# Kernel optimization log

Measured on AMD Instinct MI355X. Metric: run time of the kernel, lower is better.

## Reference

```python
import jax, jax.numpy as jnp
import numpy as np

B, S, D, H = 2, 2048, 1024, 16
DK = D // H


def setup_inputs() -> dict:
    key = jax.random.key(0)
    ks = jax.random.split(key, 12)
    s = 1.0 / np.sqrt(D)
    inp = {
        "query": jax.random.normal(ks[0], (B, S, D), jnp.float32),
        "key_": jax.random.normal(ks[1], (B, S, D), jnp.float32),
        "value": jax.random.normal(ks[2], (B, S, D), jnp.float32),
        # causal mask, broadcast over heads: [B, 1, S, S]
        "mask": jnp.broadcast_to(jnp.tril(jnp.ones((S, S), bool)), (B, 1, S, S)),
        "W_q": jax.random.uniform(ks[3], (D, D), jnp.float32, -s, s),
        "b_q": jax.random.uniform(ks[4], (D,), jnp.float32, -s, s),
        "W_k": jax.random.uniform(ks[5], (D, D), jnp.float32, -s, s),
        "b_k": jax.random.uniform(ks[6], (D,), jnp.float32, -s, s),
        "W_v": jax.random.uniform(ks[7], (D, D), jnp.float32, -s, s),
        "b_v": jax.random.uniform(ks[8], (D,), jnp.float32, -s, s),
        "W_o": jax.random.uniform(ks[9], (D, D), jnp.float32, -s, s),
        "b_o": jax.random.uniform(ks[10], (D,), jnp.float32, -s, s),
    }
    return inp


def reference(query, key_, value, mask, W_q, b_q, W_k, b_k, W_v, b_v, W_o, b_o):
    b = query.shape[0]
    # linear projections (torch Linear: x @ W.T + b)
    Q = query @ W_q.T + b_q
    K = key_ @ W_k.T + b_k
    V = value @ W_v.T + b_v
    # [b, S, H, dk] -> [b, H, S, dk]
    Q = Q.reshape(b, -1, H, DK).transpose(0, 2, 1, 3)
    K = K.reshape(b, -1, H, DK).transpose(0, 2, 1, 3)
    V = V.reshape(b, -1, H, DK).transpose(0, 2, 1, 3)
    scores = jnp.einsum("bhqd,bhkd->bhqk", Q, K) / jnp.sqrt(jnp.float32(DK))
    scores = jnp.where(mask, scores, -jnp.inf)
    attn = jax.nn.softmax(scores, axis=-1)
    out = jnp.einsum("bhqk,bhkd->bhqd", attn, V)
    out = out.transpose(0, 2, 1, 3).reshape(b, -1, D)
    return out @ W_o.T + b_o
```

## Files before the change

kernel.cpp:

```cpp
#include <hip/hip_runtime.h>
#include <hip/hip_bf16.h>
#include <stdint.h>

#define B_ 2
#define S_ 2048
#define D_ 1024
#define H_ 16
#define DK_ 64

typedef __attribute__((ext_vector_type(4))) float floatx4;
typedef __attribute__((ext_vector_type(8))) short shortx8;
typedef __attribute__((ext_vector_type(4))) short shortx4;
typedef unsigned short ushort_t;

__device__ inline ushort_t f2bf(float f) {
  union { float f; unsigned u; } v; v.f = f;
  unsigned r = v.u + 0x7FFFu + ((v.u >> 16) & 1u);
  return (ushort_t)(r >> 16);
}

__device__ inline unsigned pack2bf(float lo, float hi) {
  return __builtin_amdgcn_perm(__float_as_uint(hi), __float_as_uint(lo), 0x07060302u);
}

__device__ inline shortx4 mk_sx4(unsigned lo, unsigned hi) {
  union { unsigned u[2]; shortx4 s; } v; v.u[0] = lo; v.u[1] = hi; return v.s;
}

__device__ inline float fast_exp2(float x) {
#if __has_builtin(__builtin_amdgcn_exp2f)
  return __builtin_amdgcn_exp2f(x);
#else
  return __expf(0.69314718056f * x);
#endif
}

__device__ inline void gload_lds16(const void* g, void* l) {
  __builtin_amdgcn_global_load_lds(
      (const __attribute__((address_space(1))) unsigned int*)g,
      (__attribute__((address_space(3))) unsigned int*)l, 16, 0, 0);
}

__device__ inline floatx4 mfma16x16x16bf16(shortx4 a, shortx4 b, floatx4 c) {
#if __has_builtin(__builtin_amdgcn_mfma_f32_16x16x16bf16_1k)
  return __builtin_amdgcn_mfma_f32_16x16x16bf16_1k(a, b, c, 0, 0, 0);
#else
  floatx4 d;
  asm("v_mfma_f32_16x16x16_bf16 %0, %1, %2, %3" : "=v"(d) : "v"(a), "v"(b), "v"(c));
  return d;
#endif
}

struct ConvArgs {
  const float* src[7];
  ushort_t* dst[7];
};

__global__ __launch_bounds__(256) void convert_kernel(ConvArgs a) {
  int blk = blockIdx.x;
  int seg, bis;
  if (blk < 3072) { seg = blk >> 10; bis = blk & 1023; }
  else { int bb = blk - 3072; seg = 3 + (bb >> 8); bis = bb & 255; }
  const float4* src = (const float4*)(a.src[seg]) + (size_t)bis * 1024;
  ushort4* dst = (ushort4*)(a.dst[seg]) + (size_t)bis * 1024;
#pragma unroll
  for (int i = 0; i < 4; ++i) {
    int idx = i * 256 + threadIdx.x;
    float4 v = src[idx];
    ushort4 o;
    o.x = f2bf(v.x); o.y = f2bf(v.y); o.z = f2bf(v.z); o.w = f2bf(v.w);
    dst[idx] = o;
  }
}

template <int TM>
__device__ inline void gemm_bt_core(const ushort_t* __restrict__ A,
                                    const ushort_t* __restrict__ W,
                                    const float* __restrict__ bias,
                                    float scl,
                                    void* __restrict__ outp,
                                    int m0, int n0, int N, int K, int outmode) {
  constexpr int LDSU = (TM + 128) * 32;
  constexpr int GA = TM / 16;
  constexpr int GW = (GA + 8) / 4;
  constexpr int MI = TM / 32;
  __shared__ ushort_t smem[2][LDSU];
  const int tid = threadIdx.x;
  const int wave = tid >> 6;
  const int lane = tid & 63;
  const int quad = lane >> 4;
  const int l16 = lane & 15;
  const int wm = (wave >> 1) * (TM / 2);
  const int wn = (wave & 1) * 64;

  floatx4 acc[MI][4] = {};

  const ushort_t* gsrc[GW];
  int ldst[GW];
#pragma unroll
  for (int i = 0; i < GW; ++i) {
    int g = wave * GW + i;
    int row = lane >> 2;
    int col = (lane & 3) * 8;
    if (g < GA) {
      gsrc[i] = A + (size_t)(m0 + g * 16 + row) * K + col;
      ldst[i] = g * 512;
    } else {
      gsrc[i] = W + (size_t)(n0 + (g - GA) * 16 + row) * K + col;
      ldst[i] = TM * 32 + (g - GA) * 512;
    }
  }

#pragma unroll
  for (int i = 0; i < GW; ++i) gload_lds16(gsrc[i], &smem[0][ldst[i]]);

  const int niter = K >> 5;
  for (int j = 0; j < niter; ++j) {
    __syncthreads();
    if (j + 1 < niter) {
      const int ko = (j + 1) * 32;
      ushort_t* bufn = smem[(j + 1) & 1];
#pragma unroll
      for (int i = 0; i < GW; ++i) gload_lds16(gsrc[i] + ko, bufn + ldst[i]);
    }
    const ushort_t* aT = smem[j & 1];
    const ushort_t* bT = smem[j & 1] + TM * 32;
    shortx8 af[MI], bf[4];
#pragma unroll
    for (int mi = 0; mi < MI; ++mi)
      af[mi] = *(const shortx8*)(aT + (wm + mi * 16 + l16) * 32 + quad * 8);
#pragma unroll
    for (int ni = 0; ni < 4; ++ni)
      bf[ni] = *(const shortx8*)(bT + (wn + ni * 16 + l16) * 32 + quad * 8);
#pragma unroll
    for (int mi = 0; mi < MI; ++mi)
#pragma unroll
      for (int ni = 0; ni < 4; ++ni)
        acc[mi][ni] = __builtin_amdgcn_mfma_f32_16x16x32_bf16(af[mi], bf[ni], acc[mi][ni], 0, 0, 0);
  }

#pragma unroll
  for (int ni = 0; ni < 4; ++ni) {
    int n = n0 + wn + ni * 16 + l16;
    float bv = bias[n];
#pragma unroll
    for (int mi = 0; mi < MI; ++mi) {
      if (outmode == 2) {
        int m = m0 + wm + mi * 16 + quad * 4;
        int b = m >> 11, s = m & 2047;
        ushort_t* dst = (ushort_t*)outp + (((size_t)(b * 1024 + n)) << 11) + s;
        uint2 pk;
        pk.x = (unsigned)f2bf(acc[mi][ni][0] + bv) |
               ((unsigned)f2bf(acc[mi][ni][1] + bv) << 16);
        pk.y = (unsigned)f2bf(acc[mi][ni][2] + bv) |
               ((unsigned)f2bf(acc[mi][ni][3] + bv) << 16);
        *(uint2*)(dst) = pk;
      } else {
#pragma unroll
        for (int r = 0; r < 4; ++r) {
          int m = m0 + wm + mi * 16 + quad * 4 + r;
          float v = (acc[mi][ni][r] + bv) * scl;
          if (outmode == 1) ((float*)outp)[(size_t)m * N + n] = v;
          else ((ushort_t*)outp)[(size_t)m * N + n] = f2bf(v);
        }
      }
    }
  }
}

struct QkvArgs {
  const ushort_t* A[3];
  const ushort_t* W[3];
  const float* bias[3];
  ushort_t* out[3];
  float scale[3];
};

__global__ __launch_bounds__(256) void gemm_qkv_kernel(QkvArgs a) {
  int z = blockIdx.z;
  int m0 = (blockIdx.x * 4 + (blockIdx.y >> 3)) * 128;
  int n0 = (blockIdx.y & 7) * 128;
  gemm_bt_core<128>(a.A[z], a.W[z], a.bias[z], a.scale[z], a.out[z],
                    m0, n0, D_, D_, z == 2 ? 2 : 0);
}

__global__ __launch_bounds__(256) void gemm_out_kernel(const ushort_t* __restrict__ A,
                                                       const ushort_t* __restrict__ W,
                                                       const float* __restrict__ bias,
                                                       float* __restrict__ out) {
  int m0 = (blockIdx.x * 8 + (blockIdx.y >> 3)) * 64;
  int n0 = (blockIdx.y & 7) * 128;
  gemm_bt_core<64>(A, W, bias, 1.0f, out, m0, n0, D_, D_, 1);
}

__global__ __launch_bounds__(256, 2) void attn_kernel(const ushort_t* __restrict__ Qp,
                                                      const ushort_t* __restrict__ Kp,
                                                      const ushort_t* __restrict__ Vt,
                                                      ushort_t* __restrict__ O) {
  const int id = blockIdx.x;
  const int h = id & 15;
  const int qq = (id & 255) >> 4;
  const int b = id >> 8;
  const int qt = b ? qq : 15 - qq;
  const int q0 = qt * 128;
  const int tid = threadIdx.x;
  const int wave = tid >> 6;
  const int lane = tid & 63;
  const int quad = lane >> 4;
  const int l16 = lane & 15;

  __shared__ ushort_t smem[2][8192];

  const size_t hoff = (size_t)h * DK_;

  shortx8 qf[2][2];
#pragma unroll
  for (int grp = 0; grp < 2; ++grp) {
    const ushort_t* qrow = Qp + ((size_t)b * S_ + q0 + wave * 32 + grp * 16 + l16) * D_ + hoff;
#pragma unroll
    for (int ks = 0; ks < 2; ++ks)
      qf[grp][ks] = *(const shortx8*)(qrow + ks * 32 + quad * 8);
  }

  const int r8 = lane >> 3;
  const int jj8 = ((lane & 7) ^ r8) * 8;
  const ushort_t* kb[2];
  const ushort_t* vb[2];
#pragma unroll
  for (int g = 0; g < 2; ++g) {
    int r = wave * 16 + g * 8 + r8;
    kb[g] = Kp + ((size_t)b * S_ + r) * D_ + hoff + jj8;
    vb[g] = Vt + ((size_t)(b * H_ + h) * 64 + r) * S_ + jj8;
  }
  const int ldsrow = (wave * 16) * 64;

  floatx4 oacc[2][4] = {};
  float l_run[2] = {0.f, 0.f};
  const int nj = 2 * qt + 2;
  const int qwave_max = q0 + wave * 32 + 31;

#pragma unroll
  for (int g = 0; g < 2; ++g) {
    gload_lds16(kb[g], &smem[0][ldsrow + g * 512]);
    gload_lds16(vb[g], &smem[0][4096 + ldsrow + g * 512]);
  }

  for (int j = 0; j < nj; ++j) {
    __syncthreads();
    if (j + 1 < nj) {
      ushort_t* bufn = smem[(j + 1) & 1];
      const size_t ko = (size_t)(j + 1) * 64 * D_;
      const int vo = (j + 1) * 64;
#pragma unroll
      for (int g = 0; g < 2; ++g) {
        gload_lds16(kb[g] + ko, bufn + ldsrow + g * 512);
        gload_lds16(vb[g] + vo, bufn + 4096 + ldsrow + g * 512);
      }
    }
    if ((j << 6) > qwave_max) continue;
    const ushort_t* k_lds = smem[j & 1];
    const ushort_t* v_lds = smem[j & 1] + 4096;

    floatx4 sacc[2][4];
#pragma unroll
    for (int kkb = 0; kkb < 4; ++kkb) {
      const ushort_t* krow = k_lds + (kkb * 16 + l16) * 64;
      shortx8 af0 = *(const shortx8*)(krow + (quad ^ (l16 & 7)) * 8);
      shortx8 af1 = *(const shortx8*)(krow + ((4 | quad) ^ (l16 & 7)) * 8);
#pragma unroll
      for (int grp = 0; grp < 2; ++grp) {
        floatx4 acc = {0.f, 0.f, 0.f, 0.f};
        acc = __builtin_amdgcn_mfma_f32_16x16x32_bf16(af0, qf[grp][0], acc, 0, 0, 0);
        acc = __builtin_amdgcn_mfma_f32_16x16x32_bf16(af1, qf[grp][1], acc, 0, 0, 0);
        sacc[grp][kkb] = acc;
      }
    }
#pragma unroll
    for (int grp = 0; grp < 2; ++grp) {
      const int qg = q0 + wave * 32 + grp * 16 + l16;
      if ((j << 6) + 63 > q0 + wave * 32 + grp * 16) {
#pragma unroll
        for (int kkb = 0; kkb < 4; ++kkb)
#pragma unroll
          for (int r = 0; r < 4; ++r)
            if ((j << 6) + kkb * 16 + quad * 4 + r > qg) sacc[grp][kkb][r] = -3.0e38f;
      }
    }

    shortx4 pf[2][4];
#pragma unroll
    for (int grp = 0; grp < 2; ++grp) {
      float psum = 0.f;
#pragma unroll
      for (int kkb = 0; kkb < 4; ++kkb) {
        float p0 = fast_exp2(sacc[grp][kkb][0]);
        float p1 = fast_exp2(sacc[grp][kkb][1]);
        float p2 = fast_exp2(sacc[grp][kkb][2]);
        float p3 = fast_exp2(sacc[grp][kkb][3]);
        psum += (p0 + p1) + (p2 + p3);
        pf[grp][kkb] = mk_sx4(pack2bf(p0, p1), pack2bf(p2, p3));
      }
      l_run[grp] += psum;
    }

#pragma unroll
    for (int kkb = 0; kkb < 4; ++kkb) {
      const int jj = ((2 * kkb + (quad >> 1)) ^ (l16 & 7)) * 8 + (quad & 1) * 4;
#pragma unroll
      for (int db = 0; db < 4; ++db) {
        shortx4 vf = *(const shortx4*)(v_lds + (db * 16 + l16) * 64 + jj);
        oacc[0][db] = mfma16x16x16bf16(vf, pf[0][kkb], oacc[0][db]);
        oacc[1][db] = mfma16x16x16bf16(vf, pf[1][kkb], oacc[1][db]);
      }
    }
  }

  __syncthreads();
  ushort_t* sm = &smem[0][0];
#pragma unroll
  for (int grp = 0; grp < 2; ++grp) {
    float l0 = l_run[grp];
    l0 += __shfl_xor(l0, 16);
    l0 += __shfl_xor(l0, 32);
    float inv_l = 1.0f / l0;
    int row = wave * 32 + grp * 16 + l16;
#pragma unroll
    for (int db = 0; db < 4; ++db) {
#pragma unroll
      for (int rr = 0; rr < 2; ++rr) {
        unsigned pk = pack2bf(oacc[grp][db][rr * 2] * inv_l, oacc[grp][db][rr * 2 + 1] * inv_l);
        *(unsigned*)(sm + row * 72 + db * 16 + quad * 4 + rr * 2) = pk;
      }
    }
  }
  __syncthreads();
  {
    int r = tid >> 1, c = (tid & 1) * 32;
    const ushort_t* src = sm + r * 72 + c;
    ushort_t* dst = O + ((size_t)b * S_ + q0 + r) * D_ + hoff + c;
    uint4 v0 = *(const uint4*)(src);
    uint4 v1 = *(const uint4*)(src + 8);
    uint4 v2 = *(const uint4*)(src + 16);
    uint4 v3 = *(const uint4*)(src + 24);
    *(uint4*)(dst) = v0;
    *(uint4*)(dst + 8) = v1;
    *(uint4*)(dst + 16) = v2;
    *(uint4*)(dst + 24) = v3;
  }
}

extern "C" void kernel_launch(void* const* d_in, const int* in_sizes, int n_in,
                              void* d_out, int out_size, void* d_ws, size_t ws_size,
                              hipStream_t stream) {
  (void)in_sizes; (void)n_in; (void)out_size; (void)ws_size;
  char* ws = (char*)d_ws;
  ushort_t* xq = (ushort_t*)(ws + 0);
  ushort_t* xk = (ushort_t*)(ws + 8388608);
  ushort_t* xv = (ushort_t*)(ws + 16777216);
  ushort_t* wq = (ushort_t*)(ws + 25165824);
  ushort_t* wk = (ushort_t*)(ws + 27262976);
  ushort_t* wv = (ushort_t*)(ws + 29360128);
  ushort_t* wo = (ushort_t*)(ws + 31457280);
  ushort_t* Qp = (ushort_t*)(ws + 33554432);
  ushort_t* Kp = (ushort_t*)(ws + 41943040);
  ushort_t* Vt = (ushort_t*)(ws + 50331648);
  ushort_t* O = xq;

  ConvArgs ca;
  ca.src[0] = (const float*)d_in[0];  ca.dst[0] = xq;
  ca.src[1] = (const float*)d_in[1];  ca.dst[1] = xk;
  ca.src[2] = (const float*)d_in[2];  ca.dst[2] = xv;
  ca.src[3] = (const float*)d_in[4];  ca.dst[3] = wq;
  ca.src[4] = (const float*)d_in[6];  ca.dst[4] = wk;
  ca.src[5] = (const float*)d_in[8];  ca.dst[5] = wv;
  ca.src[6] = (const float*)d_in[10]; ca.dst[6] = wo;
  convert_kernel<<<dim3(4096), dim3(256), 0, stream>>>(ca);

  QkvArgs qa;
  qa.A[0] = xq; qa.W[0] = wq; qa.bias[0] = (const float*)d_in[5]; qa.out[0] = Qp;
  qa.A[1] = xk; qa.W[1] = wk; qa.bias[1] = (const float*)d_in[7]; qa.out[1] = Kp;
  qa.A[2] = xv; qa.W[2] = wv; qa.bias[2] = (const float*)d_in[9]; qa.out[2] = Vt;
  qa.scale[0] = 0.125f * 1.44269504089f;
  qa.scale[1] = 1.0f;
  qa.scale[2] = 1.0f;
  gemm_qkv_kernel<<<dim3(8, 32, 3), dim3(256), 0, stream>>>(qa);

  attn_kernel<<<dim3(512), dim3(256), 0, stream>>>(Qp, Kp, Vt, O);

  gemm_out_kernel<<<dim3(8, 64, 1), dim3(256), 0, stream>>>(
      O, wo, (const float*)d_in[11], (float*)d_out);
}
```

Before: 232.6 us.

## Fuse fp32-to-bf16 activation conversion into QKV GEMM loads

The QKV projection GEMM now reads the fp32 activations directly, converts them to bf16 in registers, and writes them to LDS. The separate conversion pass over the three input activation tensors is removed, leaving a smaller convert kernel that only handles the four weight matrices. This drops a full write and re-read of about 24 MB of bf16 activations. In exchange, the GEMM loads twice as many bytes for A per tile and spends VALU work on packing, and its launch bounds now ask for 3 blocks per CU. The output GEMM is specialised into a standalone kernel with the same tiling.

```diff
diff --git a/kernel.cpp b/kernel.cpp
--- a/kernel.cpp
+++ b/kernel.cpp
@@ -17,6 +17,13 @@
   union { float f; unsigned u; } v; v.f = f;
   unsigned r = v.u + 0x7FFFu + ((v.u >> 16) & 1u);
   return (ushort_t)(r >> 16);
+}
+
+__device__ inline unsigned pk_rne(float a, float b) {
+  unsigned ua = __float_as_uint(a), ub = __float_as_uint(b);
+  ua += 0x7FFFu + ((ua >> 16) & 1u);
+  ub += 0x7FFFu + ((ub >> 16) & 1u);
+  return __builtin_amdgcn_perm(ub, ua, 0x07060302u);
 }
 
 __device__ inline unsigned pack2bf(float lo, float hi) {
@@ -51,16 +58,13 @@
 #endif
 }
 
-struct ConvArgs {
-  const float* src[7];
-  ushort_t* dst[7];
+struct ConvWArgs {
+  const float* src[4];
+  ushort_t* dst[4];
 };
 
-__global__ __launch_bounds__(256) void convert_kernel(ConvArgs a) {
-  int blk = blockIdx.x;
-  int seg, bis;
-  if (blk < 3072) { seg = blk >> 10; bis = blk & 1023; }
-  else { int bb = blk - 3072; seg = 3 + (bb >> 8); bis = bb & 255; }
+__global__ __launch_bounds__(256) void convert_w_kernel(ConvWArgs a) {
+  int seg = blockIdx.x >> 8, bis = blockIdx.x & 255;
   const float4* src = (const float4*)(a.src[seg]) + (size_t)bis * 1024;
   ushort4* dst = (ushort4*)(a.dst[seg]) + (size_t)bis * 1024;
 #pragma unroll
@@ -73,70 +77,104 @@
   }
 }
 
-template <int TM>
-__device__ inline void gemm_bt_core(const ushort_t* __restrict__ A,
-                                    const ushort_t* __restrict__ W,
-                                    const float* __restrict__ bias,
-                                    float scl,
-                                    void* __restrict__ outp,
-                                    int m0, int n0, int N, int K, int outmode) {
-  constexpr int LDSU = (TM + 128) * 32;
-  constexpr int GA = TM / 16;
-  constexpr int GW = (GA + 8) / 4;
-  constexpr int MI = TM / 32;
-  __shared__ ushort_t smem[2][LDSU];
+struct QkvArgs {
+  const float* Af[3];
+  const ushort_t* W[3];
+  const float* bias[3];
+  ushort_t* out[3];
+  float scale[3];
+};
+
+__global__ __launch_bounds__(256, 3) void gemm_qkv_kernel(QkvArgs a) {
+  const int z = blockIdx.z;
+  const int m0 = (blockIdx.x * 4 + (blockIdx.y >> 3)) * 128;
+  const int n0 = (blockIdx.y & 7) * 128;
+  const float* __restrict__ A = a.Af[z];
+  const ushort_t* __restrict__ W = a.W[z];
+  const float* __restrict__ bias = a.bias[z];
+  const float scl = a.scale[z];
+  ushort_t* __restrict__ outp = a.out[z];
+  const int outmode = (z == 2) ? 2 : 0;
+  constexpr int K = D_;
+
+  __shared__ ushort_t smem[2][8192];
   const int tid = threadIdx.x;
   const int wave = tid >> 6;
   const int lane = tid & 63;
   const int quad = lane >> 4;
   const int l16 = lane & 15;
-  const int wm = (wave >> 1) * (TM / 2);
+  const int wm = (wave >> 1) * 64;
   const int wn = (wave & 1) * 64;
 
-  floatx4 acc[MI][4] = {};
-
-  const ushort_t* gsrc[GW];
-  int ldst[GW];
-#pragma unroll
-  for (int i = 0; i < GW; ++i) {
-    int g = wave * GW + i;
-    int row = lane >> 2;
-    int col = (lane & 3) * 8;
-    if (g < GA) {
-      gsrc[i] = A + (size_t)(m0 + g * 16 + row) * K + col;
-      ldst[i] = g * 512;
-    } else {
-      gsrc[i] = W + (size_t)(n0 + (g - GA) * 16 + row) * K + col;
-      ldst[i] = TM * 32 + (g - GA) * 512;
-    }
-  }
-
-#pragma unroll
-  for (int i = 0; i < GW; ++i) gload_lds16(gsrc[i], &smem[0][ldst[i]]);
-
-  const int niter = K >> 5;
-  for (int j = 0; j < niter; ++j) {
+  floatx4 acc[4][4] = {};
+
+  const ushort_t* wsrc[2];
+  int wdst[2];
+#pragma unroll
+  for (int g = 0; g < 2; ++g) {
+    int gg = wave * 2 + g;
+    wsrc[g] = W + (size_t)(n0 + gg * 16 + (lane >> 2)) * K + (lane & 3) * 8;
+    wdst[g] = 4096 + gg * 512;
+  }
+  const float* asrc0 = A + (size_t)(m0 + (tid >> 2)) * K + (tid & 3) * 8;
+  const float* asrc1 = A + (size_t)(m0 + 64 + (tid >> 2)) * K + (tid & 3) * 8;
+  const int adst0 = tid * 8;
+  const int adst1 = 2048 + tid * 8;
+
+#pragma unroll
+  for (int g = 0; g < 2; ++g) gload_lds16(wsrc[g], &smem[0][wdst[g]]);
+  {
+    float4 a0 = *(const float4*)(asrc0);
+    float4 a1 = *(const float4*)(asrc0 + 4);
+    float4 a2 = *(const float4*)(asrc1);
+    float4 a3 = *(const float4*)(asrc1 + 4);
+    uint4 p0, p1;
+    p0.x = pk_rne(a0.x, a0.y); p0.y = pk_rne(a0.z, a0.w);
+    p0.z = pk_rne(a1.x, a1.y); p0.w = pk_rne(a1.z, a1.w);
+    p1.x = pk_rne(a2.x, a2.y); p1.y = pk_rne(a2.z, a2.w);
+    p1.z = pk_rne(a3.x, a3.y); p1.w = pk_rne(a3.z, a3.w);
+    *(uint4*)(&smem[0][adst0]) = p0;
+    *(uint4*)(&smem[0][adst1]) = p1;
+  }
+
+  for (int j = 0; j < 32; ++j) {
     __syncthreads();
-    if (j + 1 < niter) {
+    float4 a0, a1, a2, a3;
+    const bool pre = (j + 1 < 32);
+    if (pre) {
       const int ko = (j + 1) * 32;
       ushort_t* bufn = smem[(j + 1) & 1];
 #pragma unroll
-      for (int i = 0; i < GW; ++i) gload_lds16(gsrc[i] + ko, bufn + ldst[i]);
+      for (int g = 0; g < 2; ++g) gload_lds16(wsrc[g] + ko, bufn + wdst[g]);
+      a0 = *(const float4*)(asrc0 + ko);
+      a1 = *(const float4*)(asrc0 + ko + 4);
+      a2 = *(const float4*)(asrc1 + ko);
+      a3 = *(const float4*)(asrc1 + ko + 4);
     }
     const ushort_t* aT = smem[j & 1];
-    const ushort_t* bT = smem[j & 1] + TM * 32;
-    shortx8 af[MI], bf[4];
-#pragma unroll
-    for (int mi = 0; mi < MI; ++mi)
+    const ushort_t* bT = smem[j & 1] + 4096;
+    shortx8 af[4], bf[4];
+#pragma unroll
+    for (int mi = 0; mi < 4; ++mi)
       af[mi] = *(const shortx8*)(aT + (wm + mi * 16 + l16) * 32 + quad * 8);
 #pragma unroll
     for (int ni = 0; ni < 4; ++ni)
       bf[ni] = *(const shortx8*)(bT + (wn + ni * 16 + l16) * 32 + quad * 8);
 #pragma unroll
-    for (int mi = 0; mi < MI; ++mi)
+    for (int mi = 0; mi < 4; ++mi)
 #pragma unroll
       for (int ni = 0; ni < 4; ++ni)
         acc[mi][ni] = __builtin_amdgcn_mfma_f32_16x16x32_bf16(af[mi], bf[ni], acc[mi][ni], 0, 0, 0);
+    if (pre) {
+      ushort_t* bufn = smem[(j + 1) & 1];
+      uint4 p0, p1;
+      p0.x = pk_rne(a0.x, a0.y); p0.y = pk_rne(a0.z, a0.w);
+      p0.z = pk_rne(a1.x, a1.y); p0.w = pk_rne(a1.z, a1.w);
+      p1.x = pk_rne(a2.x, a2.y); p1.y = pk_rne(a2.z, a2.w);
+      p1.z = pk_rne(a3.x, a3.y); p1.w = pk_rne(a3.z, a3.w);
+      *(uint4*)(bufn + adst0) = p0;
+      *(uint4*)(bufn + adst1) = p1;
+    }
   }
 
 #pragma unroll
@@ -144,11 +182,11 @@
     int n = n0 + wn + ni * 16 + l16;
     float bv = bias[n];
 #pragma unroll
-    for (int mi = 0; mi < MI; ++mi) {
+    for (int mi = 0; mi < 4; ++mi) {
       if (outmode == 2) {
         int m = m0 + wm + mi * 16 + quad * 4;
         int b = m >> 11, s = m & 2047;
-        ushort_t* dst = (ushort_t*)outp + (((size_t)(b * 1024 + n)) << 11) + s;
+        ushort_t* dst = outp + (((size_t)(b * 1024 + n)) << 11) + s;
         uint2 pk;
         pk.x = (unsigned)f2bf(acc[mi][ni][0] + bv) |
                ((unsigned)f2bf(acc[mi][ni][1] + bv) << 16);
@@ -159,38 +197,86 @@
 #pragma unroll
         for (int r = 0; r < 4; ++r) {
           int m = m0 + wm + mi * 16 + quad * 4 + r;
-          float v = (acc[mi][ni][r] + bv) * scl;
-          if (outmode == 1) ((float*)outp)[(size_t)m * N + n] = v;
-          else ((ushort_t*)outp)[(size_t)m * N + n] = f2bf(v);
+          outp[(size_t)m * D_ + n] = f2bf((acc[mi][ni][r] + bv) * scl);
         }
       }
     }
   }
-}
-
-struct QkvArgs {
-  const ushort_t* A[3];
-  const ushort_t* W[3];
-  const float* bias[3];
-  ushort_t* out[3];
-  float scale[3];
-};
-
-__global__ __launch_bounds__(256) void gemm_qkv_kernel(QkvArgs a) {
-  int z = blockIdx.z;
-  int m0 = (blockIdx.x * 4 + (blockIdx.y >> 3)) * 128;
-  int n0 = (blockIdx.y & 7) * 128;
-  gemm_bt_core<128>(a.A[z], a.W[z], a.bias[z], a.scale[z], a.out[z],
-                    m0, n0, D_, D_, z == 2 ? 2 : 0);
 }
 
 __global__ __launch_bounds__(256) void gemm_out_kernel(const ushort_t* __restrict__ A,
                                                        const ushort_t* __restrict__ W,
                                                        const float* __restrict__ bias,
                                                        float* __restrict__ out) {
-  int m0 = (blockIdx.x * 8 + (blockIdx.y >> 3)) * 64;
-  int n0 = (blockIdx.y & 7) * 128;
-  gemm_bt_core<64>(A, W, bias, 1.0f, out, m0, n0, D_, D_, 1);
+  const int m0 = (blockIdx.x * 8 + (blockIdx.y >> 3)) * 64;
+  const int n0 = (blockIdx.y & 7) * 128;
+  constexpr int K = D_;
+  __shared__ ushort_t smem[2][6144];
+  const int tid = threadIdx.x;
+  const int wave = tid >> 6;
+  const int lane = tid & 63;
+  const int quad = lane >> 4;
+  const int l16 = lane & 15;
+  const int wm = (wave >> 1) * 32;
+  const int wn = (wave & 1) * 64;
+
+  floatx4 acc[2][4] = {};
+
+  const ushort_t* gsrc[3];
+  int ldst[3];
+#pragma unroll
+  for (int i = 0; i < 3; ++i) {
+    int g = wave * 3 + i;
+    int row = lane >> 2;
+    int col = (lane & 3) * 8;
+    if (g < 4) {
+      gsrc[i] = A + (size_t)(m0 + g * 16 + row) * K + col;
+      ldst[i] = g * 512;
+    } else {
+      gsrc[i] = W + (size_t)(n0 + (g - 4) * 16 + row) * K + col;
+      ldst[i] = 2048 + (g - 4) * 512;
+    }
+  }
+
+#pragma unroll
+  for (int i = 0; i < 3; ++i) gload_lds16(gsrc[i], &smem[0][ldst[i]]);
+
+  for (int j = 0; j < 32; ++j) {
+    __syncthreads();
+    if (j + 1 < 32) {
+      const int ko = (j + 1) * 32;
+      ushort_t* bufn = smem[(j + 1) & 1];
+#pragma unroll
+      for (int i = 0; i < 3; ++i) gload_lds16(gsrc[i] + ko, bufn + ldst[i]);
+    }
+    const ushort_t* aT = smem[j & 1];
+    const ushort_t* bT = smem[j & 1] + 2048;
+    shortx8 af[2], bf[4];
+#pragma unroll
+    for (int mi = 0; mi < 2; ++mi)
+      af[mi] = *(const shortx8*)(aT + (wm + mi * 16 + l16) * 32 + quad * 8);
+#pragma unroll
+    for (int ni = 0; ni < 4; ++ni)
+      bf[ni] = *(const shortx8*)(bT + (wn + ni * 16 + l16) * 32 + quad * 8);
+#pragma unroll
+    for (int mi = 0; mi < 2; ++mi)
+#pragma unroll
+      for (int ni = 0; ni < 4; ++ni)
+        acc[mi][ni] = __builtin_amdgcn_mfma_f32_16x16x32_bf16(af[mi], bf[ni], acc[mi][ni], 0, 0, 0);
+  }
+
+#pragma unroll
+  for (int ni = 0; ni < 4; ++ni) {
+    int n = n0 + wn + ni * 16 + l16;
+    float bv = bias[n];
+#pragma unroll
+    for (int mi = 0; mi < 2; ++mi)
+#pragma unroll
+      for (int r = 0; r < 4; ++r) {
+        int m = m0 + wm + mi * 16 + quad * 4 + r;
+        out[(size_t)m * D_ + n] = acc[mi][ni][r] + bv;
+      }
+  }
 }
 
 __global__ __launch_bounds__(256, 2) void attn_kernel(const ushort_t* __restrict__ Qp,
@@ -354,9 +440,7 @@
                               hipStream_t stream) {
   (void)in_sizes; (void)n_in; (void)out_size; (void)ws_size;
   char* ws = (char*)d_ws;
-  ushort_t* xq = (ushort_t*)(ws + 0);
-  ushort_t* xk = (ushort_t*)(ws + 8388608);
-  ushort_t* xv = (ushort_t*)(ws + 16777216);
+  ushort_t* O  = (ushort_t*)(ws + 0);
   ushort_t* wq = (ushort_t*)(ws + 25165824);
   ushort_t* wk = (ushort_t*)(ws + 27262976);
   ushort_t* wv = (ushort_t*)(ws + 29360128);
@@ -364,22 +448,18 @@
   ushort_t* Qp = (ushort_t*)(ws + 33554432);
   ushort_t* Kp = (ushort_t*)(ws + 41943040);
   ushort_t* Vt = (ushort_t*)(ws + 50331648);
-  ushort_t* O = xq;
-
-  ConvArgs ca;
-  ca.src[0] = (const float*)d_in[0];  ca.dst[0] = xq;
-  ca.src[1] = (const float*)d_in[1];  ca.dst[1] = xk;
-  ca.src[2] = (const float*)d_in[2];  ca.dst[2] = xv;
-  ca.src[3] = (const float*)d_in[4];  ca.dst[3] = wq;
-  ca.src[4] = (const float*)d_in[6];  ca.dst[4] = wk;
-  ca.src[5] = (const float*)d_in[8];  ca.dst[5] = wv;
-  ca.src[6] = (const float*)d_in[10]; ca.dst[6] = wo;
-  convert_kernel<<<dim3(4096), dim3(256), 0, stream>>>(ca);
+
+  ConvWArgs cw;
+  cw.src[0] = (const float*)d_in[4];  cw.dst[0] = wq;
+  cw.src[1] = (const float*)d_in[6];  cw.dst[1] = wk;
+  cw.src[2] = (const float*)d_in[8];  cw.dst[2] = wv;
+  cw.src[3] = (const float*)d_in[10]; cw.dst[3] = wo;
+  convert_w_kernel<<<dim3(1024), dim3(256), 0, stream>>>(cw);
 
   QkvArgs qa;
-  qa.A[0] = xq; qa.W[0] = wq; qa.bias[0] = (const float*)d_in[5]; qa.out[0] = Qp;
-  qa.A[1] = xk; qa.W[1] = wk; qa.bias[1] = (const float*)d_in[7]; qa.out[1] = Kp;
-  qa.A[2] = xv; qa.W[2] = wv; qa.bias[2] = (const float*)d_in[9]; qa.out[2] = Vt;
+  qa.Af[0] = (const float*)d_in[0]; qa.W[0] = wq; qa.bias[0] = (const float*)d_in[5]; qa.out[0] = Qp;
+  qa.Af[1] = (const float*)d_in[1]; qa.W[1] = wk; qa.bias[1] = (const float*)d_in[7]; qa.out[1] = Kp;
+  qa.Af[2] = (const float*)d_in[2]; qa.W[2] = wv; qa.bias[2] = (const float*)d_in[9]; qa.out[2] = Vt;
   qa.scale[0] = 0.125f * 1.44269504089f;
   qa.scale[1] = 1.0f;
   qa.scale[2] = 1.0f;
```

Measured after the change: 240.5 us. 1.03x slower.

## Enlarge attention KV tile to 128 keys per stage with 16-way V swizzle

Applied to the files above, without the earlier changes.

Doubles the K/V block loaded into LDS per pipeline stage from 64 to 128 keys, which halves the number of loop iterations and __syncthreads barriers. Each stage is processed in two 64-key halves with causal early exit. The V tile layout is reorganized to 128-wide rows with a 16-way XOR swizzle. LDS use doubles to 64KB per block, which may limit occupancy under launch_bounds(256,2) and adds wasted loads on diagonal tiles.

```diff
diff --git a/kernel.cpp b/kernel.cpp
--- a/kernel.cpp
+++ b/kernel.cpp
@@ -209,7 +209,7 @@
   const int quad = lane >> 4;
   const int l16 = lane & 15;
 
-  __shared__ ushort_t smem[2][8192];
+  __shared__ ushort_t smem[2][16384];
 
   const size_t hoff = (size_t)h * DK_;
 
@@ -224,93 +224,104 @@
 
   const int r8 = lane >> 3;
   const int jj8 = ((lane & 7) ^ r8) * 8;
-  const ushort_t* kb[2];
-  const ushort_t* vb[2];
-#pragma unroll
-  for (int g = 0; g < 2; ++g) {
-    int r = wave * 16 + g * 8 + r8;
+  const ushort_t* kb[4];
+#pragma unroll
+  for (int g = 0; g < 4; ++g) {
+    int r = wave * 32 + g * 8 + r8;
     kb[g] = Kp + ((size_t)b * S_ + r) * D_ + hoff + jj8;
-    vb[g] = Vt + ((size_t)(b * H_ + h) * 64 + r) * S_ + jj8;
-  }
-  const int ldsrow = (wave * 16) * 64;
+  }
+  const int r4 = lane >> 4;
+  const ushort_t* vb[4];
+#pragma unroll
+  for (int g = 0; g < 4; ++g) {
+    int r = wave * 16 + g * 4 + r4;
+    int cpos = ((lane & 15) ^ ((g * 4 + r4) & 15)) * 8;
+    vb[g] = Vt + ((size_t)(b * H_ + h) * 64 + r) * S_ + cpos;
+  }
 
   floatx4 oacc[2][4] = {};
   float l_run[2] = {0.f, 0.f};
-  const int nj = 2 * qt + 2;
+  const int nj = qt + 1;
   const int qwave_max = q0 + wave * 32 + 31;
 
 #pragma unroll
-  for (int g = 0; g < 2; ++g) {
-    gload_lds16(kb[g], &smem[0][ldsrow + g * 512]);
-    gload_lds16(vb[g], &smem[0][4096 + ldsrow + g * 512]);
+  for (int g = 0; g < 4; ++g) {
+    gload_lds16(kb[g], &smem[0][wave * 2048 + g * 512]);
+    gload_lds16(vb[g], &smem[0][8192 + wave * 2048 + g * 512]);
   }
 
   for (int j = 0; j < nj; ++j) {
     __syncthreads();
     if (j + 1 < nj) {
       ushort_t* bufn = smem[(j + 1) & 1];
-      const size_t ko = (size_t)(j + 1) * 64 * D_;
-      const int vo = (j + 1) * 64;
-#pragma unroll
-      for (int g = 0; g < 2; ++g) {
-        gload_lds16(kb[g] + ko, bufn + ldsrow + g * 512);
-        gload_lds16(vb[g] + vo, bufn + 4096 + ldsrow + g * 512);
-      }
-    }
-    if ((j << 6) > qwave_max) continue;
+      const size_t ko = (size_t)(j + 1) * 128 * D_;
+      const int vo = (j + 1) * 128;
+#pragma unroll
+      for (int g = 0; g < 4; ++g) {
+        gload_lds16(kb[g] + ko, bufn + wave * 2048 + g * 512);
+        gload_lds16(vb[g] + vo, bufn + 8192 + wave * 2048 + g * 512);
+      }
+    }
+    if (j * 128 > qwave_max) continue;
     const ushort_t* k_lds = smem[j & 1];
-    const ushort_t* v_lds = smem[j & 1] + 4096;
-
-    floatx4 sacc[2][4];
-#pragma unroll
-    for (int kkb = 0; kkb < 4; ++kkb) {
-      const ushort_t* krow = k_lds + (kkb * 16 + l16) * 64;
-      shortx8 af0 = *(const shortx8*)(krow + (quad ^ (l16 & 7)) * 8);
-      shortx8 af1 = *(const shortx8*)(krow + ((4 | quad) ^ (l16 & 7)) * 8);
+    const ushort_t* v_lds = smem[j & 1] + 8192;
+
+#pragma unroll
+    for (int half = 0; half < 2; ++half) {
+      const int kbase = j * 128 + half * 64;
+      if (kbase > qwave_max) break;
+
+      floatx4 sacc[2][4];
+#pragma unroll
+      for (int kkb = 0; kkb < 4; ++kkb) {
+        const ushort_t* krow = k_lds + (half * 64 + kkb * 16 + l16) * 64;
+        shortx8 af0 = *(const shortx8*)(krow + (quad ^ (l16 & 7)) * 8);
+        shortx8 af1 = *(const shortx8*)(krow + ((4 | quad) ^ (l16 & 7)) * 8);
+#pragma unroll
+        for (int grp = 0; grp < 2; ++grp) {
+          floatx4 acc = {0.f, 0.f, 0.f, 0.f};
+          acc = __builtin_amdgcn_mfma_f32_16x16x32_bf16(af0, qf[grp][0], acc, 0, 0, 0);
+          acc = __builtin_amdgcn_mfma_f32_16x16x32_bf16(af1, qf[grp][1], acc, 0, 0, 0);
+          sacc[grp][kkb] = acc;
+        }
+      }
 #pragma unroll
       for (int grp = 0; grp < 2; ++grp) {
-        floatx4 acc = {0.f, 0.f, 0.f, 0.f};
-        acc = __builtin_amdgcn_mfma_f32_16x16x32_bf16(af0, qf[grp][0], acc, 0, 0, 0);
-        acc = __builtin_amdgcn_mfma_f32_16x16x32_bf16(af1, qf[grp][1], acc, 0, 0, 0);
-        sacc[grp][kkb] = acc;
-      }
-    }
-#pragma unroll
-    for (int grp = 0; grp < 2; ++grp) {
-      const int qg = q0 + wave * 32 + grp * 16 + l16;
-      if ((j << 6) + 63 > q0 + wave * 32 + grp * 16) {
-#pragma unroll
-        for (int kkb = 0; kkb < 4; ++kkb)
-#pragma unroll
-          for (int r = 0; r < 4; ++r)
-            if ((j << 6) + kkb * 16 + quad * 4 + r > qg) sacc[grp][kkb][r] = -3.0e38f;
-      }
-    }
-
-    shortx4 pf[2][4];
-#pragma unroll
-    for (int grp = 0; grp < 2; ++grp) {
-      float psum = 0.f;
+        const int qg = q0 + wave * 32 + grp * 16 + l16;
+        if (kbase + 63 > q0 + wave * 32 + grp * 16) {
+#pragma unroll
+          for (int kkb = 0; kkb < 4; ++kkb)
+#pragma unroll
+            for (int r = 0; r < 4; ++r)
+              if (kbase + kkb * 16 + quad * 4 + r > qg) sacc[grp][kkb][r] = -3.0e38f;
+        }
+      }
+
+      shortx4 pf[2][4];
+#pragma unroll
+      for (int grp = 0; grp < 2; ++grp) {
+        float psum = 0.f;
+#pragma unroll
+        for (int kkb = 0; kkb < 4; ++kkb) {
+          float p0 = fast_exp2(sacc[grp][kkb][0]);
+          float p1 = fast_exp2(sacc[grp][kkb][1]);
+          float p2 = fast_exp2(sacc[grp][kkb][2]);
+          float p3 = fast_exp2(sacc[grp][kkb][3]);
+          psum += (p0 + p1) + (p2 + p3);
+          pf[grp][kkb] = mk_sx4(pack2bf(p0, p1), pack2bf(p2, p3));
+        }
+        l_run[grp] += psum;
+      }
+
 #pragma unroll
       for (int kkb = 0; kkb < 4; ++kkb) {
-        float p0 = fast_exp2(sacc[grp][kkb][0]);
-        float p1 = fast_exp2(sacc[grp][kkb][1]);
-        float p2 = fast_exp2(sacc[grp][kkb][2]);
-        float p3 = fast_exp2(sacc[grp][kkb][3]);
-        psum += (p0 + p1) + (p2 + p3);
-        pf[grp][kkb] = mk_sx4(pack2bf(p0, p1), pack2bf(p2, p3));
-      }
-      l_run[grp] += psum;
-    }
-
-#pragma unroll
-    for (int kkb = 0; kkb < 4; ++kkb) {
-      const int jj = ((2 * kkb + (quad >> 1)) ^ (l16 & 7)) * 8 + (quad & 1) * 4;
-#pragma unroll
-      for (int db = 0; db < 4; ++db) {
-        shortx4 vf = *(const shortx4*)(v_lds + (db * 16 + l16) * 64 + jj);
-        oacc[0][db] = mfma16x16x16bf16(vf, pf[0][kkb], oacc[0][db]);
-        oacc[1][db] = mfma16x16x16bf16(vf, pf[1][kkb], oacc[1][db]);
+        const int jj = ((half * 8 + kkb * 2 + (quad >> 1)) ^ l16) * 8 + (quad & 1) * 4;
+#pragma unroll
+        for (int db = 0; db < 4; ++db) {
+          shortx4 vf = *(const shortx4*)(v_lds + (db * 16 + l16) * 128 + jj);
+          oacc[0][db] = mfma16x16x16bf16(vf, pf[0][kkb], oacc[0][db]);
+          oacc[1][db] = mfma16x16x16bf16(vf, pf[1][kkb], oacc[1][db]);
+        }
       }
     }
   }
```

New measurement: 227.7 us. 2.1% less time.
